# Performance work log

Hardware: AMD Instinct MI355X
Metric: run time of the kernel (lower is better)

The kernel has to match this reference:

```python
import jax, jax.numpy as jnp
import numpy as np

N_NODES = 50000
N_EDGES = 1200000
N_GRAPHS = 512
GC_COUNT = 3
CUTOFF = 8.0
BN_EPS = 1e-5
LOG2 = float(np.log(2.0))


def ssp(v):
    # ShiftedSoftplus
    return jax.nn.softplus(v) - LOG2


def setup_inputs() -> dict:
    key = jax.random.key(0)
    ks = jax.random.split(key, 16)
    d1, nf, ng = 64, 92, 50
    inp = {}
    inp["x"] = jax.random.normal(ks[0], (N_NODES, nf), dtype=jnp.float32)
    # distances in [0, cutoff)
    inp["edge_weight"] = jax.random.uniform(ks[1], (N_EDGES,), dtype=jnp.float32) * CUTOFF
    inp["edge_attr"] = jax.random.normal(ks[2], (N_EDGES, ng), dtype=jnp.float32)
    inp["edge_index"] = jax.random.randint(ks[3], (2, N_EDGES), 0, N_NODES, dtype=jnp.int32)
    inp["batch"] = jnp.sort(jax.random.randint(ks[4], (N_NODES,), 0, N_GRAPHS, dtype=jnp.int32))
    s = lambda fan_in: 1.0 / np.sqrt(fan_in)
    inp["pre_W"] = jax.random.normal(ks[5], (d1, nf), dtype=jnp.float32) * s(nf)
    inp["pre_b"] = jnp.zeros((d1,), jnp.float32)
    inp["mlp_W1"] = jax.random.normal(ks[6], (GC_COUNT, d1, ng), dtype=jnp.float32) * s(ng)
    inp["mlp_b1"] = jnp.zeros((GC_COUNT, d1), jnp.float32)
    inp["mlp_W2"] = jax.random.normal(ks[7], (GC_COUNT, d1, d1), dtype=jnp.float32) * s(d1)
    inp["mlp_b2"] = jnp.zeros((GC_COUNT, d1), jnp.float32)
    inp["cf_W1"] = jax.random.normal(ks[8], (GC_COUNT, d1, d1), dtype=jnp.float32) * s(d1)
    inp["cf_W2"] = jax.random.normal(ks[9], (GC_COUNT, d1, d1), dtype=jnp.float32) * s(d1)
    inp["cf_b2"] = jnp.zeros((GC_COUNT, d1), jnp.float32)
    inp["int_W"] = jax.random.normal(ks[10], (GC_COUNT, d1, d1), dtype=jnp.float32) * s(d1)
    inp["int_b"] = jnp.zeros((GC_COUNT, d1), jnp.float32)
    inp["bn_g"] = jnp.ones((GC_COUNT, d1), jnp.float32)
    inp["bn_b"] = jnp.zeros((GC_COUNT, d1), jnp.float32)
    inp["post_W"] = jax.random.normal(ks[11], (d1, d1), dtype=jnp.float32) * s(d1)
    inp["post_b"] = jnp.zeros((d1,), jnp.float32)
    inp["out_W"] = jax.random.normal(ks[12], (1, d1), dtype=jnp.float32) * s(d1)
    inp["out_b"] = jnp.zeros((1,), jnp.float32)
    return inp


def reference(x, edge_weight, edge_attr, edge_index, batch,
              pre_W, pre_b, mlp_W1, mlp_b1, mlp_W2, mlp_b2,
              cf_W1, cf_W2, cf_b2, int_W, int_b, bn_g, bn_b,
              post_W, post_b, out_W, out_b):
    src, dst = edge_index[0], edge_index[1]
    # pre FC
    out = jax.nn.relu(x @ pre_W.T + pre_b)
    # cosine cutoff on edge distances, shared across layers
    C = 0.5 * (jnp.cos(edge_weight * (jnp.pi / CUTOFF)) + 1.0)  # [E]
    for l in range(GC_COUNT):
        # filter-generating MLP on edge_attr, modulated by cutoff
        W = ssp(edge_attr @ mlp_W1[l].T + mlp_b1[l]) @ mlp_W2[l].T + mlp_b2[l]
        W = W * C[:, None]  # [E, F]
        # CFConv: lin1 -> gather -> modulate -> scatter-add -> lin2
        h = out @ cf_W1[l].T                      # [N, F]
        msg = h[src] * W                          # [E, F]
        agg = jax.ops.segment_sum(msg, dst, num_segments=N_NODES)  # [N, F]
        h = agg @ cf_W2[l].T + cf_b2[l]
        # InteractionBlock tail: act + lin
        h = ssp(h) @ int_W[l].T + int_b[l]
        out = out + h
        # BatchNorm1d (training mode: batch statistics, biased variance)
        mu = jnp.mean(out, axis=0)
        var = jnp.mean((out - mu) ** 2, axis=0)
        out = (out - mu) * jax.lax.rsqrt(var + BN_EPS) * bn_g[l] + bn_b[l]
    # global_mean_pool over graphs
    sums = jax.ops.segment_sum(out, batch, num_segments=N_GRAPHS)  # [G, F]
    counts = jax.ops.segment_sum(jnp.ones((out.shape[0],), out.dtype), batch, num_segments=N_GRAPHS)
    pooled = sums / jnp.maximum(counts, 1.0)[:, None]
    # post FC + head
    h = jax.nn.relu(pooled @ post_W.T + post_b)
    y = h @ out_W.T + out_b  # [G, 1]
    return y.reshape(-1)
```

## Files before the change

kernel.cpp:

```cpp
#include <hip/hip_runtime.h>

constexpr int N = 50000;
constexpr int E = 1200000;
constexpr int G = 512;
constexpr int TILES = E / 64;
constexpr float LOG2_ = 0.69314718055994531f;
constexpr float PIC = 0.39269908169872414f;

typedef __attribute__((ext_vector_type(8))) short s8;
typedef __attribute__((ext_vector_type(4))) float f32x4;

__device__ __forceinline__ float sspf(float x) {
    return fmaxf(x, 0.f) + __logf(1.f + __expf(-fabsf(x))) - LOG2_;
}
__device__ __forceinline__ void uadd(float* p, float v) { unsafeAtomicAdd(p, v); }
__device__ __forceinline__ ushort bf16rne(float x) {
    unsigned u = __float_as_uint(x);
    return (ushort)((u + 0x7FFFu + ((u >> 16) & 1u)) >> 16);
}
__device__ __forceinline__ float bf2f(ushort h) {
    return __uint_as_float(((unsigned)h) << 16);
}

__global__ __launch_bounds__(256) void k_hist(const int* __restrict__ eidx,
                                              int* __restrict__ cnt) {
    for (int e = blockIdx.x * 256 + threadIdx.x; e < E; e += gridDim.x * 256)
        atomicAdd(cnt + eidx[E + e], 1);
}

__global__ __launch_bounds__(1024) void k_scan(const int* __restrict__ cnt,
                                               int* __restrict__ cursor) {
    __shared__ int part[1024];
    const int CH = 49;
    int t = threadIdx.x;
    int b = t * CH;
    int s = 0;
    for (int i = 0; i < CH; i++) { int idx = b + i; if (idx < N) s += cnt[idx]; }
    part[t] = s;
    __syncthreads();
    for (int off = 1; off < 1024; off <<= 1) {
        int add = (t >= off) ? part[t - off] : 0;
        int v = part[t];
        __syncthreads();
        part[t] = v + add;
        __syncthreads();
    }
    int excl = (t == 0) ? 0 : part[t - 1];
    for (int i = 0; i < CH; i++) {
        int idx = b + i;
        if (idx < N) { cursor[idx] = excl; excl += cnt[idx]; }
    }
}

__global__ __launch_bounds__(256) void k_scatter(const int* __restrict__ eidx,
                                                 int* __restrict__ cursor,
                                                 int* __restrict__ order,
                                                 int* __restrict__ rank) {
    for (int e = blockIdx.x * 256 + threadIdx.x; e < E; e += gridDim.x * 256) {
        int d = eidx[E + e];
        int p = atomicAdd(cursor + d, 1);
        order[p] = e;
        rank[e] = p;
    }
}

__global__ __launch_bounds__(256) void k_meta(const int* __restrict__ eidx,
                                              const float* __restrict__ ew,
                                              const int* __restrict__ rank,
                                              int* __restrict__ srcs,
                                              int* __restrict__ dsts,
                                              float* __restrict__ Cs) {
    for (int e = blockIdx.x * 256 + threadIdx.x; e < E; e += gridDim.x * 256) {
        int p = rank[e];
        srcs[p] = eidx[e];
        dsts[p] = eidx[E + e];
        Cs[p] = 0.5f * (cosf(ew[e] * PIC) + 1.0f);
    }
}

__global__ __launch_bounds__(256) void k_pack(const float* __restrict__ W1,
                                              const float* __restrict__ W2,
                                              ushort* __restrict__ wpk) {
    int l = blockIdx.x;
    ushort* o = wpk + l * 16384;
    for (int idx = threadIdx.x; idx < 4096; idx += 256) {
        int j = idx & 7, f = (idx >> 3) & 63, g = (idx >> 9) & 3, ks = idx >> 11;
        int k = ks * 32 + g * 8 + j;
        float v1 = (k < 50) ? W1[l * 3200 + f * 50 + k] : 0.f;
        ushort h1 = bf16rne(v1);
        o[idx] = h1;
        o[4096 + idx] = bf16rne(v1 - bf2f(h1));
        float v2 = W2[l * 4096 + f * 64 + k];
        ushort h2 = bf16rne(v2);
        o[8192 + idx] = h2;
        o[12288 + idx] = bf16rne(v2 - bf2f(h2));
    }
}

__global__ __launch_bounds__(256) void k_pre(const float* __restrict__ x,
                                             const float* __restrict__ W,
                                             const float* __restrict__ b,
                                             float* __restrict__ out) {
    __shared__ float WT[92 * 64];
    __shared__ float xs[4 * 92];
    __shared__ float bs[64];
    for (int i = threadIdx.x; i < 92 * 64; i += 256) {
        int f = i / 92, k = i - f * 92;
        WT[k * 64 + f] = W[i];
    }
    if (threadIdx.x < 64) bs[threadIdx.x] = b[threadIdx.x];
    __syncthreads();
    int f = threadIdx.x & 63, nl = threadIdx.x >> 6;
    for (int g0 = blockIdx.x; g0 < N / 4; g0 += gridDim.x) {
        int n0 = g0 * 4;
        for (int i = threadIdx.x; i < 4 * 92; i += 256) xs[i] = x[(size_t)n0 * 92 + i];
        __syncthreads();
        float acc = bs[f];
        #pragma unroll 4
        for (int k = 0; k < 92; k++) acc = fmaf(xs[nl * 92 + k], WT[k * 64 + f], acc);
        out[(size_t)(n0 + nl) * 64 + f] = fmaxf(acc, 0.f);
        __syncthreads();
    }
}

__global__ __launch_bounds__(256) void k_h(float* __restrict__ out,
                                           const float* __restrict__ W,
                                           const float* __restrict__ bnacc,
                                           int useBN,
                                           float* __restrict__ h) {
    __shared__ float WT[64 * 64];
    __shared__ float xs[4 * 64];
    int t = threadIdx.x;
    for (int i = t; i < 4096; i += 256) {
        int f = i >> 6, j = i & 63;
        WT[j * 64 + f] = W[i];
    }
    float4 sc = make_float4(1.f, 1.f, 1.f, 1.f);
    float4 sh = make_float4(0.f, 0.f, 0.f, 0.f);
    if (t < 64 && useBN) {
        sc = ((const float4*)(bnacc + 128))[t & 15];
        sh = ((const float4*)(bnacc + 192))[t & 15];
    }
    __syncthreads();
    int f = t & 63, nl = t >> 6;
    for (int g0 = blockIdx.x; g0 < N / 4; g0 += gridDim.x) {
        int n0 = g0 * 4;
        if (t < 64) {
            float4 v = ((const float4*)(out + (size_t)n0 * 64))[t];
            v.x = fmaf(v.x, sc.x, sh.x);
            v.y = fmaf(v.y, sc.y, sh.y);
            v.z = fmaf(v.z, sc.z, sh.z);
            v.w = fmaf(v.w, sc.w, sh.w);
            ((float4*)xs)[t] = v;
            if (useBN) ((float4*)(out + (size_t)n0 * 64))[t] = v;
        }
        __syncthreads();
        float acc = 0.f;
        #pragma unroll 4
        for (int j = 0; j < 64; j++) acc = fmaf(xs[nl * 64 + j], WT[j * 64 + f], acc);
        h[(size_t)(n0 + nl) * 64 + f] = acc;
        __syncthreads();
    }
}

__global__ __launch_bounds__(256, 2) void k_edge1(const float* __restrict__ ea,
                                                  const float* __restrict__ ew,
                                                  const int* __restrict__ rank,
                                                  float* __restrict__ wfc,
                                                  const ushort* __restrict__ wpk_l,
                                                  const float* __restrict__ b1,
                                                  const float* __restrict__ b2) {
    __shared__ ushort eaH[4096], eaL[4096];
    __shared__ ushort t1H[4096], t1L[4096];
    __shared__ float  bufB[64 * 68];

    const int t = threadIdx.x;
    const int w = t >> 6, l = t & 63;
    const int lm = l & 15, lg = l >> 4;
    const int se = t & 63, sq = t >> 6;
    const int e4 = (t & 15) * 4, f4 = (t >> 4) * 4;
    const int erow = w * 16 + lm;

    s8 b1h[4][2], b1l[4][2], b2h[4][2], b2l[4][2];
    #pragma unroll
    for (int ft = 0; ft < 4; ft++)
        #pragma unroll
        for (int ks = 0; ks < 2; ks++) {
            int idx = ((ks * 4 + lg) * 64 + ft * 16 + lm) * 8;
            b1h[ft][ks] = *(const s8*)(wpk_l + idx);
            b1l[ft][ks] = *(const s8*)(wpk_l + 4096 + idx);
            b2h[ft][ks] = *(const s8*)(wpk_l + 8192 + idx);
            b2l[ft][ks] = *(const s8*)(wpk_l + 12288 + idx);
        }
    float b1v[4], b2v[4];
    #pragma unroll
    for (int ft = 0; ft < 4; ft++) { b1v[ft] = b1[ft * 16 + lm]; b2v[ft] = b2[ft * 16 + lm]; }

    for (int tile = blockIdx.x; tile < TILES; tile += gridDim.x) {
        const int e0 = tile * 64;
        float pv[16];
        {
            const float* row = ea + (size_t)(e0 + se) * 50;
            if (sq < 3) {
                #pragma unroll
                for (int i = 0; i < 8; i++) {
                    float2 v = *(const float2*)(row + sq * 16 + i * 2);
                    pv[2 * i] = v.x; pv[2 * i + 1] = v.y;
                }
            } else {
                float2 v = *(const float2*)(row + 48);
                pv[0] = v.x; pv[1] = v.y;
                #pragma unroll
                for (int i = 2; i < 16; i++) pv[i] = 0.f;
            }
        }
        float4 ew4 = *(const float4*)&ew[e0 + w * 16 + lg * 4];
        float cvr[4] = {0.5f * (__cosf(ew4.x * PIC) + 1.0f),
                        0.5f * (__cosf(ew4.y * PIC) + 1.0f),
                        0.5f * (__cosf(ew4.z * PIC) + 1.0f),
                        0.5f * (__cosf(ew4.w * PIC) + 1.0f)};
        int4 rk4 = *(const int4*)&rank[e0 + e4];
        __syncthreads();
        #pragma unroll
        for (int c2 = 0; c2 < 2; c2++) {
            int swz = (sq * 2 + c2) ^ (se & 7);
            s8 hi, lo;
            #pragma unroll
            for (int j = 0; j < 8; j++) {
                float x = pv[c2 * 8 + j];
                ushort hh = bf16rne(x);
                hi[j] = (short)hh;
                lo[j] = (short)bf16rne(x - bf2f(hh));
            }
            *(s8*)&eaH[se * 64 + swz * 8] = hi;
            *(s8*)&eaL[se * 64 + swz * 8] = lo;
        }
        __syncthreads();
        f32x4 acc[4];
        #pragma unroll
        for (int ft = 0; ft < 4; ft++) acc[ft] = (f32x4){b1v[ft], b1v[ft], b1v[ft], b1v[ft]};
        #pragma unroll
        for (int ks = 0; ks < 2; ks++) {
            int swz = (ks * 4 + lg) ^ (erow & 7);
            s8 ah = *(const s8*)&eaH[erow * 64 + swz * 8];
            s8 al = *(const s8*)&eaL[erow * 64 + swz * 8];
            #pragma unroll
            for (int ft = 0; ft < 4; ft++) {
                acc[ft] = __builtin_amdgcn_mfma_f32_16x16x32_bf16(ah, b1h[ft][ks], acc[ft], 0, 0, 0);
                acc[ft] = __builtin_amdgcn_mfma_f32_16x16x32_bf16(ah, b1l[ft][ks], acc[ft], 0, 0, 0);
                acc[ft] = __builtin_amdgcn_mfma_f32_16x16x32_bf16(al, b1h[ft][ks], acc[ft], 0, 0, 0);
            }
        }
        #pragma unroll
        for (int ft = 0; ft < 4; ft++) {
            int k = ft * 16 + lm;
            int cbase = k >> 3;
            #pragma unroll
            for (int r = 0; r < 4; r++) {
                int eR = w * 16 + lg * 4 + r;
                float v = sspf(acc[ft][r]);
                ushort hh = bf16rne(v);
                ushort ll = bf16rne(v - bf2f(hh));
                int idx = eR * 64 + ((cbase ^ (eR & 7)) << 3) + (k & 7);
                t1H[idx] = hh;
                t1L[idx] = ll;
            }
        }
        __syncthreads();
        f32x4 acc2[4];
        #pragma unroll
        for (int ft = 0; ft < 4; ft++) acc2[ft] = (f32x4){b2v[ft], b2v[ft], b2v[ft], b2v[ft]};
        #pragma unroll
        for (int ks = 0; ks < 2; ks++) {
            int swz = (ks * 4 + lg) ^ (erow & 7);
            s8 ah = *(const s8*)&t1H[erow * 64 + swz * 8];
            s8 al = *(const s8*)&t1L[erow * 64 + swz * 8];
            #pragma unroll
            for (int ft = 0; ft < 4; ft++) {
                acc2[ft] = __builtin_amdgcn_mfma_f32_16x16x32_bf16(ah, b2h[ft][ks], acc2[ft], 0, 0, 0);
                acc2[ft] = __builtin_amdgcn_mfma_f32_16x16x32_bf16(ah, b2l[ft][ks], acc2[ft], 0, 0, 0);
                acc2[ft] = __builtin_amdgcn_mfma_f32_16x16x32_bf16(al, b2h[ft][ks], acc2[ft], 0, 0, 0);
            }
        }
        #pragma unroll
        for (int ft = 0; ft < 4; ft++) {
            int f = ft * 16 + lm;
            #pragma unroll
            for (int r = 0; r < 4; r++) {
                int eR = w * 16 + lg * 4 + r;
                bufB[eR * 68 + f] = acc2[ft][r] * cvr[r];
            }
        }
        __syncthreads();
        {
            float4 v0 = *(const float4*)&bufB[(e4 + 0) * 68 + f4];
            float4 v1 = *(const float4*)&bufB[(e4 + 1) * 68 + f4];
            float4 v2 = *(const float4*)&bufB[(e4 + 2) * 68 + f4];
            float4 v3 = *(const float4*)&bufB[(e4 + 3) * 68 + f4];
            *(float4*)&wfc[(size_t)rk4.x * 64 + f4] = v0;
            *(float4*)&wfc[(size_t)rk4.y * 64 + f4] = v1;
            *(float4*)&wfc[(size_t)rk4.z * 64 + f4] = v2;
            *(float4*)&wfc[(size_t)rk4.w * 64 + f4] = v3;
        }
    }
}

__global__ __launch_bounds__(256) void k_edge2(const float* __restrict__ wfc,
                                               const int* __restrict__ srcs,
                                               const int* __restrict__ dsts,
                                               const float* __restrict__ h,
                                               float* __restrict__ agg) {
    __shared__ float bufB[64 * 68];
    __shared__ int dstS[64];
    const int t = threadIdx.x;
    const int e4 = (t & 15) * 4, f4 = (t >> 4) * 4;
    for (int tile = blockIdx.x; tile < TILES; tile += gridDim.x) {
        const int e0 = tile * 64;
        int dreg = 0;
        if (t < 64) dreg = dsts[e0 + t];
        int4 srcv = *(const int4*)&srcs[e0 + e4];
        float4 hv0 = *(const float4*)&h[(size_t)srcv.x * 64 + f4];
        float4 hv1 = *(const float4*)&h[(size_t)srcv.y * 64 + f4];
        float4 hv2 = *(const float4*)&h[(size_t)srcv.z * 64 + f4];
        float4 hv3 = *(const float4*)&h[(size_t)srcv.w * 64 + f4];
        __syncthreads();
        const float4* src4 = (const float4*)(wfc + (size_t)e0 * 64);
        #pragma unroll
        for (int k2 = 0; k2 < 4; k2++) {
            int idx = t + k2 * 256;
            int e = idx >> 4, fq = idx & 15;
            *(float4*)&bufB[e * 68 + fq * 4] = src4[idx];
        }
        if (t < 64) dstS[t] = dreg;
        __syncthreads();
        {
            float4* p0 = (float4*)&bufB[(e4 + 0) * 68 + f4];
            float4* p1 = (float4*)&bufB[(e4 + 1) * 68 + f4];
            float4* p2 = (float4*)&bufB[(e4 + 2) * 68 + f4];
            float4* p3 = (float4*)&bufB[(e4 + 3) * 68 + f4];
            float4 m0 = *p0, m1 = *p1, m2 = *p2, m3 = *p3;
            m0.x *= hv0.x; m0.y *= hv0.y; m0.z *= hv0.z; m0.w *= hv0.w;
            m1.x *= hv1.x; m1.y *= hv1.y; m1.z *= hv1.z; m1.w *= hv1.w;
            m2.x *= hv2.x; m2.y *= hv2.y; m2.z *= hv2.z; m2.w *= hv2.w;
            m3.x *= hv3.x; m3.y *= hv3.y; m3.z *= hv3.z; m3.w *= hv3.w;
            *p0 = m0; *p1 = m1; *p2 = m2; *p3 = m3;
        }
        __syncthreads();
        #pragma unroll
        for (int i = 0; i < 4; i++) {
            int e = e4 + i;
            int d = dstS[e];
            if (e > 0 && dstS[e - 1] == d) continue;
            int end = e + 1;
            while (end < 64 && dstS[end] == d) end++;
            float4 s = *(const float4*)&bufB[e * 68 + f4];
            for (int r = e + 1; r < end; r++) {
                float4 v = *(const float4*)&bufB[r * 68 + f4];
                s.x += v.x; s.y += v.y; s.z += v.z; s.w += v.w;
            }
            float* ap = agg + (size_t)d * 64 + f4;
            if (e > 0 && end < 64) {
                *(float4*)ap = s;
            } else {
                uadd(ap + 0, s.x); uadd(ap + 1, s.y);
                uadd(ap + 2, s.z); uadd(ap + 3, s.w);
            }
        }
    }
}

__global__ __launch_bounds__(256) void k_edgeC(const float* __restrict__ ea,
                                               const int* __restrict__ order,
                                               const int* __restrict__ srcs,
                                               const int* __restrict__ dsts,
                                               const float* __restrict__ Cs,
                                               const float* __restrict__ h,
                                               float* __restrict__ agg,
                                               const float* __restrict__ W1,
                                               const float* __restrict__ b1,
                                               const float* __restrict__ W2,
                                               const float* __restrict__ b2) {
    constexpr int BS = 68;
    __shared__ float w1T[50 * 64];
    __shared__ float w2T[64 * 64];
    __shared__ float buf[64 * BS];
    __shared__ float b1s[64], b2s[64], c_s[64];
    __shared__ int src_s[64], dst_s[64], ord_s[64];
    int t = threadIdx.x;
    for (int i = t; i < 3200; i += 256) { int f = i / 50, k = i - f * 50; w1T[k * 64 + f] = W1[i]; }
    for (int i = t; i < 4096; i += 256) { int f = i >> 6, j = i & 63; w2T[j * 64 + f] = W2[i]; }
    if (t < 64) { b1s[t] = b1[t]; b2s[t] = b2[t]; }
    __syncthreads();
    const int e4 = (t & 15) * 4;
    const int f4 = (t >> 4) * 4;
    const int fe = t & 63, kq = t >> 6;
    for (int tile = blockIdx.x; tile < TILES; tile += gridDim.x) {
        const int e0 = tile * 64;
        if (t < 64) {
            ord_s[t] = order[e0 + t];
            src_s[t] = srcs[e0 + t];
            dst_s[t] = dsts[e0 + t];
            c_s[t] = Cs[e0 + t];
        }
        __syncthreads();
        {
            const float2* row2 = (const float2*)ea + (size_t)ord_s[fe] * 25;
            #pragma unroll
            for (int j = 0; j < 24; j += 4) {
                int kp = j + kq;
                float2 v = row2[kp];
                buf[(2 * kp) * BS + fe] = v.x;
                buf[(2 * kp + 1) * BS + fe] = v.y;
            }
            if (kq == 0) {
                float2 v = row2[24];
                buf[48 * BS + fe] = v.x;
                buf[49 * BS + fe] = v.y;
            }
        }
        __syncthreads();
        float a[4][4];
        #pragma unroll
        for (int i = 0; i < 4; i++)
            #pragma unroll
            for (int j = 0; j < 4; j++) a[i][j] = b1s[f4 + j];
        #pragma unroll 2
        for (int k = 0; k < 50; k++) {
            float4 av = *(const float4*)&buf[k * BS + e4];
            float4 wv = *(const float4*)&w1T[k * 64 + f4];
            float avv[4] = {av.x, av.y, av.z, av.w};
            float wvv[4] = {wv.x, wv.y, wv.z, wv.w};
            #pragma unroll
            for (int i = 0; i < 4; i++)
                #pragma unroll
                for (int j = 0; j < 4; j++) a[i][j] = fmaf(avv[i], wvv[j], a[i][j]);
        }
        #pragma unroll
        for (int i = 0; i < 4; i++)
            #pragma unroll
            for (int j = 0; j < 4; j++) a[i][j] = sspf(a[i][j]);
        __syncthreads();
        #pragma unroll
        for (int j = 0; j < 4; j++)
            *(float4*)&buf[(f4 + j) * BS + e4] = make_float4(a[0][j], a[1][j], a[2][j], a[3][j]);
        __syncthreads();
        float w[4][4];
        #pragma unroll
        for (int i = 0; i < 4; i++)
            #pragma unroll
            for (int j = 0; j < 4; j++) w[i][j] = b2s[f4 + j];
        #pragma unroll 2
        for (int k = 0; k < 64; k++) {
            float4 tv = *(const float4*)&buf[k * BS + e4];
            float4 wv = *(const float4*)&w2T[k * 64 + f4];
            float tvv[4] = {tv.x, tv.y, tv.z, tv.w};
            float wvv[4] = {wv.x, wv.y, wv.z, wv.w};
            #pragma unroll
            for (int i = 0; i < 4; i++)
                #pragma unroll
                for (int j = 0; j < 4; j++) w[i][j] = fmaf(tvv[i], wvv[j], w[i][j]);
        }
        float4 m[4];
        #pragma unroll
        for (int i = 0; i < 4; i++) {
            int eg = e4 + i;
            float Cv = c_s[eg];
            float4 hv = *(const float4*)&h[(size_t)src_s[eg] * 64 + f4];
            m[i] = make_float4(hv.x * w[i][0] * Cv, hv.y * w[i][1] * Cv,
                               hv.z * w[i][2] * Cv, hv.w * w[i][3] * Cv);
        }
        __syncthreads();
        #pragma unroll
        for (int i = 0; i < 4; i++)
            *(float4*)&buf[(e4 + i) * BS + f4] = m[i];
        __syncthreads();
        #pragma unroll
        for (int i = 0; i < 4; i++) {
            int e = e4 + i;
            int d = dst_s[e];
            if (e > 0 && dst_s[e - 1] == d) continue;
            int end = e + 1;
            while (end < 64 && dst_s[end] == d) end++;
            float4 s = *(const float4*)&buf[e * BS + f4];
            for (int r = e + 1; r < end; r++) {
                const float4 v = *(const float4*)&buf[r * BS + f4];
                s.x += v.x; s.y += v.y; s.z += v.z; s.w += v.w;
            }
            float* ap = agg + (size_t)d * 64 + f4;
            if (e > 0 && end < 64) {
                *(float4*)ap = s;
            } else {
                uadd(ap + 0, s.x); uadd(ap + 1, s.y);
                uadd(ap + 2, s.z); uadd(ap + 3, s.w);
            }
        }
        __syncthreads();
    }
}

__global__ __launch_bounds__(256) void k_post(const float* __restrict__ agg,
                                              const float* __restrict__ W2c,
                                              const float* __restrict__ b2c,
                                              const float* __restrict__ Wi,
                                              const float* __restrict__ bi,
                                              float* __restrict__ out,
                                              float* __restrict__ bnacc) {
    __shared__ float w2T[64 * 64];
    __shared__ float wiT[64 * 64];
    __shared__ float aL[16 * 64];
    __shared__ float sL[16 * 64];
    __shared__ float b2s[64], bis[64];
    int t = threadIdx.x;
    for (int i = t; i < 4096; i += 256) {
        int f = i >> 6, j = i & 63;
        w2T[j * 64 + f] = W2c[i];
        wiT[j * 64 + f] = Wi[i];
    }
    if (t < 64) { b2s[t] = b2c[t]; bis[t] = bi[t]; }
    __syncthreads();
    const int nl = t >> 4;
    const int f4 = (t & 15) * 4;
    for (int g0 = blockIdx.x; g0 < N / 16; g0 += gridDim.x) {
        int n0 = g0 * 16;
        ((float4*)aL)[t] = ((const float4*)(agg + (size_t)n0 * 64))[t];
        __syncthreads();
        float s[4] = {b2s[f4], b2s[f4 + 1], b2s[f4 + 2], b2s[f4 + 3]};
        #pragma unroll 4
        for (int j = 0; j < 64; j++) {
            float av = aL[nl * 64 + j];
            float4 wv = *(const float4*)&w2T[j * 64 + f4];
            s[0] = fmaf(av, wv.x, s[0]);
            s[1] = fmaf(av, wv.y, s[1]);
            s[2] = fmaf(av, wv.z, s[2]);
            s[3] = fmaf(av, wv.w, s[3]);
        }
        #pragma unroll
        for (int j = 0; j < 4; j++) s[j] = sspf(s[j]);
        *(float4*)&sL[nl * 64 + f4] = make_float4(s[0], s[1], s[2], s[3]);
        __syncthreads();
        float h2[4] = {bis[f4], bis[f4 + 1], bis[f4 + 2], bis[f4 + 3]};
        #pragma unroll 4
        for (int j = 0; j < 64; j++) {
            float sv = sL[nl * 64 + j];
            float4 wv = *(const float4*)&wiT[j * 64 + f4];
            h2[0] = fmaf(sv, wv.x, h2[0]);
            h2[1] = fmaf(sv, wv.y, h2[1]);
            h2[2] = fmaf(sv, wv.z, h2[2]);
            h2[3] = fmaf(sv, wv.w, h2[3]);
        }
        float4 ov = *(const float4*)&out[(size_t)(n0 + nl) * 64 + f4];
        ov.x += h2[0]; ov.y += h2[1]; ov.z += h2[2]; ov.w += h2[3];
        *(float4*)&out[(size_t)(n0 + nl) * 64 + f4] = ov;
        *(float4*)&aL[nl * 64 + f4] = ov;
        __syncthreads();
        if (t < 64) {
            float sm = 0.f, s2 = 0.f;
            #pragma unroll 4
            for (int n = 0; n < 16; n++) {
                float v = aL[n * 64 + t];
                sm += v;
                s2 = fmaf(v, v, s2);
            }
            uadd(bnacc + t, sm);
            uadd(bnacc + 64 + t, s2);
        }
        __syncthreads();
    }
}

__global__ void k_bnfin(float* bnacc, const float* __restrict__ g, const float* __restrict__ b) {
    int f = threadIdx.x;
    double mu = (double)bnacc[f] / (double)N;
    double var = (double)bnacc[64 + f] / (double)N - mu * mu;
    double inv = 1.0 / sqrt(var + 1e-5);
    double sc = (double)g[f] * inv;
    bnacc[128 + f] = (float)sc;
    bnacc[192 + f] = (float)((double)b[f] - mu * sc);
}

__global__ __launch_bounds__(256) void k_pool(const float* __restrict__ out,
                                              const int* __restrict__ batch,
                                              const float* __restrict__ bnacc,
                                              float* __restrict__ psum,
                                              float* __restrict__ pcnt) {
    int t = threadIdx.x;
    int q = blockIdx.x * 16 + (t >> 4);
    if (q >= N / 4) return;
    int c = t & 15;
    float4 sc = ((const float4*)(bnacc + 128))[c];
    float4 sh = ((const float4*)(bnacc + 192))[c];
    int n0 = q * 4;
    int gprev = batch[n0];
    float4 acc = {0.f, 0.f, 0.f, 0.f};
    float cnt = 0.f;
    for (int i = 0; i < 4; i++) {
        int n = n0 + i;
        int gb = batch[n];
        float4 v = ((const float4*)(out + (size_t)n * 64))[c];
        v.x = fmaf(v.x, sc.x, sh.x);
        v.y = fmaf(v.y, sc.y, sh.y);
        v.z = fmaf(v.z, sc.z, sh.z);
        v.w = fmaf(v.w, sc.w, sh.w);
        if (gb != gprev) {
            float* p = psum + (size_t)gprev * 64 + c * 4;
            uadd(p + 0, acc.x); uadd(p + 1, acc.y); uadd(p + 2, acc.z); uadd(p + 3, acc.w);
            if (c == 0) uadd(pcnt + gprev, cnt);
            acc = make_float4(0.f, 0.f, 0.f, 0.f);
            cnt = 0.f;
            gprev = gb;
        }
        acc.x += v.x; acc.y += v.y; acc.z += v.z; acc.w += v.w;
        cnt += 1.f;
    }
    float* p = psum + (size_t)gprev * 64 + c * 4;
    uadd(p + 0, acc.x); uadd(p + 1, acc.y); uadd(p + 2, acc.z); uadd(p + 3, acc.w);
    if (c == 0) uadd(pcnt + gprev, cnt);
}

__global__ __launch_bounds__(256) void k_head(const float* __restrict__ psum,
                                              const float* __restrict__ pcnt,
                                              const float* __restrict__ pW,
                                              const float* __restrict__ pb,
                                              const float* __restrict__ oW,
                                              const float* __restrict__ ob,
                                              float* __restrict__ y) {
    __shared__ float pl[4][64];
    int t = threadIdx.x;
    int gl = t >> 6, f = t & 63;
    int g = blockIdx.x * 4 + gl;
    float cnt = fmaxf(pcnt[g], 1.f);
    pl[gl][f] = psum[(size_t)g * 64 + f] / cnt;
    __syncthreads();
    float acc = pb[f];
    #pragma unroll 4
    for (int j = 0; j < 64; j++) acc = fmaf(pl[gl][j], pW[f * 64 + j], acc);
    float hh = fmaxf(acc, 0.f);
    float part = hh * oW[f];
    #pragma unroll
    for (int off = 32; off; off >>= 1) part += __shfl_xor(part, off);
    if (f == 0) y[g] = part + ob[0];
}

extern "C" void kernel_launch(void* const* d_in, const int* in_sizes, int n_in,
                              void* d_out, int out_size, void* d_ws, size_t ws_size,
                              hipStream_t stream) {
    const float* x      = (const float*)d_in[0];
    const float* ew     = (const float*)d_in[1];
    const float* ea     = (const float*)d_in[2];
    const int*   eidx   = (const int*)d_in[3];
    const int*   batch  = (const int*)d_in[4];
    const float* pre_W  = (const float*)d_in[5];
    const float* pre_b  = (const float*)d_in[6];
    const float* mlp_W1 = (const float*)d_in[7];
    const float* mlp_b1 = (const float*)d_in[8];
    const float* mlp_W2 = (const float*)d_in[9];
    const float* mlp_b2 = (const float*)d_in[10];
    const float* cf_W1  = (const float*)d_in[11];
    const float* cf_W2  = (const float*)d_in[12];
    const float* cf_b2  = (const float*)d_in[13];
    const float* int_W  = (const float*)d_in[14];
    const float* int_b  = (const float*)d_in[15];
    const float* bn_g   = (const float*)d_in[16];
    const float* bn_b   = (const float*)d_in[17];
    const float* post_W = (const float*)d_in[18];
    const float* post_b = (const float*)d_in[19];
    const float* out_W  = (const float*)d_in[20];
    const float* out_b  = (const float*)d_in[21];

    float* ws    = (float*)d_ws;
    float* outb  = ws;
    float* hb    = ws + (size_t)N * 64;
    float* aggb  = ws + (size_t)2 * N * 64;
    float* bnacc = ws + (size_t)3 * N * 64;
    float* psum  = bnacc + 256;
    float* pcnt  = psum + (size_t)G * 64;
    int*   cnt   = (int*)(pcnt + G);
    int*   curs  = cnt + N;
    int*   order = curs + N;
    int*   rank  = order + E;
    int*   srcs  = rank + E;
    int*   dsts  = srcs + E;
    float* Csrt  = (float*)(dsts + E);
    ushort* wpk  = (ushort*)(Csrt + E);
    float* wfc   = (float*)(wpk + 3 * 16384);

    size_t needA = (size_t)((char*)wfc - (char*)d_ws) + (size_t)E * 64 * sizeof(float);
    const bool pathA = (ws_size >= needA);

    hipMemsetAsync(cnt, 0, (size_t)N * sizeof(int), stream);
    k_hist<<<1024, 256, 0, stream>>>(eidx, cnt);
    k_scan<<<1, 1024, 0, stream>>>(cnt, curs);
    k_scatter<<<2048, 256, 0, stream>>>(eidx, curs, order, rank);
    k_meta<<<2048, 256, 0, stream>>>(eidx, ew, rank, srcs, dsts, Csrt);
    if (pathA) k_pack<<<3, 256, 0, stream>>>(mlp_W1, mlp_W2, wpk);

    k_pre<<<1024, 256, 0, stream>>>(x, pre_W, pre_b, outb);

    for (int l = 0; l < 3; l++) {
        hipMemsetAsync(aggb, 0, (size_t)N * 64 * sizeof(float), stream);
        k_h<<<1024, 256, 0, stream>>>(outb, cf_W1 + l * 4096, bnacc, l > 0 ? 1 : 0, hb);
        hipMemsetAsync(bnacc, 0, 128 * sizeof(float), stream);
        if (pathA) {
            k_edge1<<<1024, 256, 0, stream>>>(ea, ew, rank, wfc,
                                              wpk + l * 16384, mlp_b1 + l * 64, mlp_b2 + l * 64);
            k_edge2<<<2048, 256, 0, stream>>>(wfc, srcs, dsts, hb, aggb);
        } else {
            k_edgeC<<<1536, 256, 0, stream>>>(ea, order, srcs, dsts, Csrt, hb, aggb,
                                              mlp_W1 + l * 3200, mlp_b1 + l * 64,
                                              mlp_W2 + l * 4096, mlp_b2 + l * 64);
        }
        k_post<<<1024, 256, 0, stream>>>(aggb, cf_W2 + l * 4096, cf_b2 + l * 64,
                                         int_W + l * 4096, int_b + l * 64, outb, bnacc);
        k_bnfin<<<1, 64, 0, stream>>>(bnacc, bn_g + l * 64, bn_b + l * 64);
    }

    hipMemsetAsync(psum, 0, (size_t)(G * 64 + G) * sizeof(float), stream);
    k_pool<<<(N / 4 + 15) / 16, 256, 0, stream>>>(outb, batch, bnacc, psum, pcnt);
    k_head<<<G / 4, 256, 0, stream>>>(psum, pcnt, post_W, post_b, out_W, out_b, (float*)d_out);
}
```

Before: 2.178 ms.

## Pre-split edge attributes once and fuse edge MLP with gather-scatter

A one-time kernel reorders edge attributes into destination-sorted order and stores them as pre-swizzled bf16 hi/lo tiles. Each layer then runs a single fused edge kernel. It computes the filter MLP, multiplies by the gathered source features and scatters into the aggregate, and it prefetches the next tile's attributes into registers while the current tile is processed. This removes the per-layer E×64 float intermediate write and read, and repeating the bf16 split three times. The cost is a larger workspace for the packed attributes and higher register pressure, now that the occupancy hint of 2 blocks per SM has been dropped.

```diff
diff --git a/kernel.cpp b/kernel.cpp
--- a/kernel.cpp
+++ b/kernel.cpp
@@ -75,6 +75,45 @@
         srcs[p] = eidx[e];
         dsts[p] = eidx[E + e];
         Cs[p] = 0.5f * (cosf(ew[e] * PIC) + 1.0f);
+    }
+}
+
+__global__ __launch_bounds__(256) void k_gea(const float* __restrict__ ea,
+                                             const int* __restrict__ rank,
+                                             ushort* __restrict__ eapk) {
+    for (int idx = blockIdx.x * 256 + threadIdx.x; idx < E * 4; idx += gridDim.x * 256) {
+        int e = idx >> 2, q = idx & 3;
+        int p = rank[e];
+        int T = p >> 6, se = p & 63;
+        ushort* hbase = eapk + (size_t)T * 8192 + se * 64;
+        const float* row = ea + (size_t)e * 50;
+        float v[16];
+        if (q < 3) {
+            #pragma unroll
+            for (int i = 0; i < 8; i++) {
+                float2 x = *(const float2*)(row + q * 16 + i * 2);
+                v[2 * i] = x.x; v[2 * i + 1] = x.y;
+            }
+        } else {
+            float2 x = *(const float2*)(row + 48);
+            v[0] = x.x; v[1] = x.y;
+            #pragma unroll
+            for (int i = 2; i < 16; i++) v[i] = 0.f;
+        }
+        #pragma unroll
+        for (int c2 = 0; c2 < 2; c2++) {
+            int swz = ((q * 2 + c2) ^ (se & 7)) * 8;
+            s8 hi, lo;
+            #pragma unroll
+            for (int j = 0; j < 8; j++) {
+                float x = v[c2 * 8 + j];
+                ushort hh = bf16rne(x);
+                hi[j] = (short)hh;
+                lo[j] = (short)bf16rne(x - bf2f(hh));
+            }
+            *(s8*)(hbase + swz) = hi;
+            *(s8*)(hbase + 4096 + swz) = lo;
+        }
     }
 }
 
@@ -163,21 +202,23 @@
     }
 }
 
-__global__ __launch_bounds__(256, 2) void k_edge1(const float* __restrict__ ea,
-                                                  const float* __restrict__ ew,
-                                                  const int* __restrict__ rank,
-                                                  float* __restrict__ wfc,
-                                                  const ushort* __restrict__ wpk_l,
-                                                  const float* __restrict__ b1,
-                                                  const float* __restrict__ b2) {
-    __shared__ ushort eaH[4096], eaL[4096];
+__global__ __launch_bounds__(256) void k_edge(const ushort* __restrict__ eapk,
+                                              const int* __restrict__ srcs,
+                                              const int* __restrict__ dsts,
+                                              const float* __restrict__ Cs,
+                                              const float* __restrict__ h,
+                                              float* __restrict__ agg,
+                                              const ushort* __restrict__ wpk_l,
+                                              const float* __restrict__ b1,
+                                              const float* __restrict__ b2) {
+    __shared__ ushort eaT[8192];
     __shared__ ushort t1H[4096], t1L[4096];
     __shared__ float  bufB[64 * 68];
+    __shared__ int    dstS[64];
 
     const int t = threadIdx.x;
     const int w = t >> 6, l = t & 63;
     const int lm = l & 15, lg = l >> 4;
-    const int se = t & 63, sq = t >> 6;
     const int e4 = (t & 15) * 4, f4 = (t >> 4) * 4;
     const int erow = w * 16 + lm;
 
@@ -196,54 +237,36 @@
     #pragma unroll
     for (int ft = 0; ft < 4; ft++) { b1v[ft] = b1[ft * 16 + lm]; b2v[ft] = b2[ft * 16 + lm]; }
 
+    {
+        const s8* g = (const s8*)(eapk + (size_t)blockIdx.x * 8192);
+        #pragma unroll
+        for (int k = 0; k < 4; k++)
+            *(s8*)&eaT[(t + k * 256) * 8] = g[t + k * 256];
+    }
+    __syncthreads();
+
     for (int tile = blockIdx.x; tile < TILES; tile += gridDim.x) {
         const int e0 = tile * 64;
-        float pv[16];
-        {
-            const float* row = ea + (size_t)(e0 + se) * 50;
-            if (sq < 3) {
-                #pragma unroll
-                for (int i = 0; i < 8; i++) {
-                    float2 v = *(const float2*)(row + sq * 16 + i * 2);
-                    pv[2 * i] = v.x; pv[2 * i + 1] = v.y;
-                }
-            } else {
-                float2 v = *(const float2*)(row + 48);
-                pv[0] = v.x; pv[1] = v.y;
-                #pragma unroll
-                for (int i = 2; i < 16; i++) pv[i] = 0.f;
-            }
-        }
-        float4 ew4 = *(const float4*)&ew[e0 + w * 16 + lg * 4];
-        float cvr[4] = {0.5f * (__cosf(ew4.x * PIC) + 1.0f),
-                        0.5f * (__cosf(ew4.y * PIC) + 1.0f),
-                        0.5f * (__cosf(ew4.z * PIC) + 1.0f),
-                        0.5f * (__cosf(ew4.w * PIC) + 1.0f)};
-        int4 rk4 = *(const int4*)&rank[e0 + e4];
-        __syncthreads();
-        #pragma unroll
-        for (int c2 = 0; c2 < 2; c2++) {
-            int swz = (sq * 2 + c2) ^ (se & 7);
-            s8 hi, lo;
-            #pragma unroll
-            for (int j = 0; j < 8; j++) {
-                float x = pv[c2 * 8 + j];
-                ushort hh = bf16rne(x);
-                hi[j] = (short)hh;
-                lo[j] = (short)bf16rne(x - bf2f(hh));
-            }
-            *(s8*)&eaH[se * 64 + swz * 8] = hi;
-            *(s8*)&eaL[se * 64 + swz * 8] = lo;
-        }
-        __syncthreads();
+        int ntile = tile + gridDim.x;
+        const s8* gnext = (const s8*)(eapk + (size_t)(ntile < TILES ? ntile : tile) * 8192);
+        s8 pv0 = gnext[t], pv1 = gnext[t + 256], pv2 = gnext[t + 512], pv3 = gnext[t + 768];
+        int4 srcv = *(const int4*)&srcs[e0 + e4];
+        float4 cv4 = *(const float4*)&Cs[e0 + w * 16 + lg * 4];
+        float4 hv0 = *(const float4*)&h[(size_t)srcv.x * 64 + f4];
+        float4 hv1 = *(const float4*)&h[(size_t)srcv.y * 64 + f4];
+        float4 hv2 = *(const float4*)&h[(size_t)srcv.z * 64 + f4];
+        float4 hv3 = *(const float4*)&h[(size_t)srcv.w * 64 + f4];
+        int dreg = 0;
+        if (t < 64) dreg = dsts[e0 + t];
+
         f32x4 acc[4];
         #pragma unroll
         for (int ft = 0; ft < 4; ft++) acc[ft] = (f32x4){b1v[ft], b1v[ft], b1v[ft], b1v[ft]};
         #pragma unroll
         for (int ks = 0; ks < 2; ks++) {
             int swz = (ks * 4 + lg) ^ (erow & 7);
-            s8 ah = *(const s8*)&eaH[erow * 64 + swz * 8];
-            s8 al = *(const s8*)&eaL[erow * 64 + swz * 8];
+            s8 ah = *(const s8*)&eaT[erow * 64 + swz * 8];
+            s8 al = *(const s8*)&eaT[4096 + erow * 64 + swz * 8];
             #pragma unroll
             for (int ft = 0; ft < 4; ft++) {
                 acc[ft] = __builtin_amdgcn_mfma_f32_16x16x32_bf16(ah, b1h[ft][ks], acc[ft], 0, 0, 0);
@@ -267,6 +290,12 @@
             }
         }
         __syncthreads();
+        *(s8*)&eaT[(t + 0 * 256) * 8] = pv0;
+        *(s8*)&eaT[(t + 1 * 256) * 8] = pv1;
+        *(s8*)&eaT[(t + 2 * 256) * 8] = pv2;
+        *(s8*)&eaT[(t + 3 * 256) * 8] = pv3;
+        if (t < 64) dstS[t] = dreg;
+
         f32x4 acc2[4];
         #pragma unroll
         for (int ft = 0; ft < 4; ft++) acc2[ft] = (f32x4){b2v[ft], b2v[ft], b2v[ft], b2v[ft]};
@@ -282,6 +311,7 @@
                 acc2[ft] = __builtin_amdgcn_mfma_f32_16x16x32_bf16(al, b2h[ft][ks], acc2[ft], 0, 0, 0);
             }
         }
+        float cvr[4] = {cv4.x, cv4.y, cv4.z, cv4.w};
         #pragma unroll
         for (int ft = 0; ft < 4; ft++) {
             int f = ft * 16 + lm;
@@ -291,47 +321,6 @@
                 bufB[eR * 68 + f] = acc2[ft][r] * cvr[r];
             }
         }
-        __syncthreads();
-        {
-            float4 v0 = *(const float4*)&bufB[(e4 + 0) * 68 + f4];
-            float4 v1 = *(const float4*)&bufB[(e4 + 1) * 68 + f4];
-            float4 v2 = *(const float4*)&bufB[(e4 + 2) * 68 + f4];
-            float4 v3 = *(const float4*)&bufB[(e4 + 3) * 68 + f4];
-            *(float4*)&wfc[(size_t)rk4.x * 64 + f4] = v0;
-            *(float4*)&wfc[(size_t)rk4.y * 64 + f4] = v1;
-            *(float4*)&wfc[(size_t)rk4.z * 64 + f4] = v2;
-            *(float4*)&wfc[(size_t)rk4.w * 64 + f4] = v3;
-        }
-    }
-}
-
-__global__ __launch_bounds__(256) void k_edge2(const float* __restrict__ wfc,
-                                               const int* __restrict__ srcs,
-                                               const int* __restrict__ dsts,
-                                               const float* __restrict__ h,
-                                               float* __restrict__ agg) {
-    __shared__ float bufB[64 * 68];
-    __shared__ int dstS[64];
-    const int t = threadIdx.x;
-    const int e4 = (t & 15) * 4, f4 = (t >> 4) * 4;
-    for (int tile = blockIdx.x; tile < TILES; tile += gridDim.x) {
-        const int e0 = tile * 64;
-        int dreg = 0;
-        if (t < 64) dreg = dsts[e0 + t];
-        int4 srcv = *(const int4*)&srcs[e0 + e4];
-        float4 hv0 = *(const float4*)&h[(size_t)srcv.x * 64 + f4];
-        float4 hv1 = *(const float4*)&h[(size_t)srcv.y * 64 + f4];
-        float4 hv2 = *(const float4*)&h[(size_t)srcv.z * 64 + f4];
-        float4 hv3 = *(const float4*)&h[(size_t)srcv.w * 64 + f4];
-        __syncthreads();
-        const float4* src4 = (const float4*)(wfc + (size_t)e0 * 64);
-        #pragma unroll
-        for (int k2 = 0; k2 < 4; k2++) {
-            int idx = t + k2 * 256;
-            int e = idx >> 4, fq = idx & 15;
-            *(float4*)&bufB[e * 68 + fq * 4] = src4[idx];
-        }
-        if (t < 64) dstS[t] = dreg;
         __syncthreads();
         {
             float4* p0 = (float4*)&bufB[(e4 + 0) * 68 + f4];
@@ -682,9 +671,9 @@
     int*   dsts  = srcs + E;
     float* Csrt  = (float*)(dsts + E);
     ushort* wpk  = (ushort*)(Csrt + E);
-    float* wfc   = (float*)(wpk + 3 * 16384);
-
-    size_t needA = (size_t)((char*)wfc - (char*)d_ws) + (size_t)E * 64 * sizeof(float);
+    ushort* eapk = wpk + 3 * 16384;
+
+    size_t needA = (size_t)((char*)(eapk + (size_t)TILES * 8192) - (char*)d_ws);
     const bool pathA = (ws_size >= needA);
 
     hipMemsetAsync(cnt, 0, (size_t)N * sizeof(int), stream);
@@ -692,7 +681,10 @@
     k_scan<<<1, 1024, 0, stream>>>(cnt, curs);
     k_scatter<<<2048, 256, 0, stream>>>(eidx, curs, order, rank);
     k_meta<<<2048, 256, 0, stream>>>(eidx, ew, rank, srcs, dsts, Csrt);
-    if (pathA) k_pack<<<3, 256, 0, stream>>>(mlp_W1, mlp_W2, wpk);
+    if (pathA) {
+        k_gea<<<2048, 256, 0, stream>>>(ea, rank, eapk);
+        k_pack<<<3, 256, 0, stream>>>(mlp_W1, mlp_W2, wpk);
+    }
 
     k_pre<<<1024, 256, 0, stream>>>(x, pre_W, pre_b, outb);
 
@@ -701,9 +693,8 @@
         k_h<<<1024, 256, 0, stream>>>(outb, cf_W1 + l * 4096, bnacc, l > 0 ? 1 : 0, hb);
         hipMemsetAsync(bnacc, 0, 128 * sizeof(float), stream);
         if (pathA) {
-            k_edge1<<<1024, 256, 0, stream>>>(ea, ew, rank, wfc,
-                                              wpk + l * 16384, mlp_b1 + l * 64, mlp_b2 + l * 64);
-            k_edge2<<<2048, 256, 0, stream>>>(wfc, srcs, dsts, hb, aggb);
+            k_edge<<<1024, 256, 0, stream>>>(eapk, srcs, dsts, Csrt, hb, aggb,
+                                             wpk + l * 16384, mlp_b1 + l * 64, mlp_b2 + l * 64);
         } else {
             k_edgeC<<<1536, 256, 0, stream>>>(ea, order, srcs, dsts, Csrt, hb, aggb,
                                               mlp_W1 + l * 3200, mlp_b1 + l * 64,
```

New measurement: 3.429 ms. 57.5% more time.
